# Kernel optimization log

Measured on AMD Instinct MI355X. Metric: run time of the kernel, lower is better.

The kernel has to match this reference:

```python
import jax, jax.numpy as jnp
import numpy as np

N_NODES = 20000
BN_EPS = 1e-5


def setup_inputs() -> dict:
    key = jax.random.key(0)
    ks = jax.random.split(key, 8)
    in_dim, half, out_dim, n_edges = 256, 128, 256, 320000
    s = 1.0 / np.sqrt(in_dim)
    return {
        "x": jax.random.normal(ks[0], (N_NODES, in_dim), dtype=jnp.float32),
        "edge_index": jax.random.randint(ks[1], (2, n_edges), 0, N_NODES, dtype=jnp.int64),
        "W_l_f": jax.random.normal(ks[2], (half, in_dim), dtype=jnp.float32) * s,
        "b_l_f": jnp.zeros((half,), dtype=jnp.float32),
        "W_r_f": jax.random.normal(ks[3], (half, in_dim), dtype=jnp.float32) * s,
        "W_l_b": jax.random.normal(ks[4], (half, in_dim), dtype=jnp.float32) * s,
        "b_l_b": jnp.zeros((half,), dtype=jnp.float32),
        "W_r_b": jax.random.normal(ks[5], (half, in_dim), dtype=jnp.float32) * s,
        "gamma": jnp.ones((out_dim,), dtype=jnp.float32),
        "beta": jnp.zeros((out_dim,), dtype=jnp.float32),
    }


def _sage(x, src, dst, W_l, b_l, W_r):
    # mean-aggregate source features at destination nodes (PyG SAGEConv, aggr='mean')
    msg_sum = jax.ops.segment_sum(x[src], dst, num_segments=N_NODES)
    cnt = jax.ops.segment_sum(jnp.ones((src.shape[0],), x.dtype), dst, num_segments=N_NODES)
    aggr = msg_sum / jnp.maximum(cnt, 1.0)[:, None]
    # lin_l(aggr) + lin_r(x); lin_l carries the bias in PyG
    return aggr @ W_l.T + b_l + x @ W_r.T


def reference(x, edge_index, W_l_f, b_l_f, W_r_f, W_l_b, b_l_b, W_r_b, gamma, beta):
    src, dst = edge_index[0], edge_index[1]
    h_fwd = _sage(x, src, dst, W_l_f, b_l_f, W_r_f)
    h_bwd = _sage(x, dst, src, W_l_b, b_l_b, W_r_b)  # flipped edges
    h = jnp.concatenate([h_fwd, h_bwd], axis=-1)  # [N, out_dim]
    # BatchNorm1d in training mode (N > 1), biased variance
    mean = jnp.mean(h, axis=0)
    var = jnp.mean(jnp.square(h - mean), axis=0)
    h = (h - mean) * jax.lax.rsqrt(var + BN_EPS) * gamma + beta
    return jax.nn.relu(h)
```

## Files before the change

### kernel.cpp

```cpp
#include <hip/hip_runtime.h>
#include <hip/hip_bf16.h>

#define N_NODES 20000
#define N_EDGES 320000
#define BN_EPS  1e-5f

#define GEMM_MT  ((N_NODES + 127) / 128)
#define NGEMM    (GEMM_MT * 4)
#define FILLB    625

typedef __attribute__((ext_vector_type(4))) float f32x4;
typedef __attribute__((ext_vector_type(8))) __bf16 bf16x8;
typedef __attribute__((ext_vector_type(4))) unsigned short u16x4;

__device__ __forceinline__ unsigned short f2bf(float f) {
    unsigned int u = __float_as_uint(f);
    u += 0x7fffu + ((u >> 16) & 1u);
    return (unsigned short)(u >> 16);
}
__device__ __forceinline__ float bflo(unsigned int u) { return __uint_as_float(u << 16); }
__device__ __forceinline__ float bfhi(unsigned int u) { return __uint_as_float(u & 0xffff0000u); }

__device__ __forceinline__ void gload_lds16(const void* g, void* l) {
    __builtin_amdgcn_global_load_lds(
        (const __attribute__((address_space(1))) void*)g,
        (__attribute__((address_space(3))) void*)l, 16, 0, 0);
}

__global__ __launch_bounds__(256) void cvt_zero_kernel(
    const float* __restrict__ x,
    const float* __restrict__ Wlf, const float* __restrict__ Wlb,
    const float* __restrict__ Wrf, const float* __restrict__ Wrb,
    unsigned short* __restrict__ Xb, unsigned short* __restrict__ Wb,
    uint4* __restrict__ zp, int zquads)
{
    const int XQ = N_NODES * 256 / 4;
    const int WQ = 128 * 256 / 4;
    const int total = XQ + 4 * WQ + zquads;
    for (int i = blockIdx.x * blockDim.x + threadIdx.x; i < total; i += gridDim.x * blockDim.x) {
        if (i >= XQ + 4 * WQ) {
            zp[i - XQ - 4 * WQ] = make_uint4(0, 0, 0, 0);
            continue;
        }
        const float* sp;
        unsigned short* dp;
        if (i < XQ) {
            sp = x + (size_t)i * 4;
            dp = Xb + (size_t)i * 4;
        } else {
            int w = i - XQ;
            int mat = w / WQ;
            int o = (w - mat * WQ) * 4;
            if      (mat == 0) sp = Wlf + o;
            else if (mat == 1) sp = Wlb + o;
            else if (mat == 2) sp = Wrf + o;
            else               sp = Wrb + o;
            dp = Wb + (size_t)mat * 32768 + o;
        }
        float4 v = *(const float4*)sp;
        u16x4 r = {f2bf(v.x), f2bf(v.y), f2bf(v.z), f2bf(v.w)};
        *(u16x4*)dp = r;
    }
}

__global__ void count_rank_kernel(const int* __restrict__ src, const int* __restrict__ dst,
                                  int* __restrict__ cntF, int* __restrict__ cntB,
                                  unsigned int* __restrict__ rank2) {
    int e = blockIdx.x * blockDim.x + threadIdx.x;
    if (e < N_EDGES) {
        unsigned int p = (unsigned int)atomicAdd(&cntF[dst[e]], 1);
        unsigned int q = (unsigned int)atomicAdd(&cntB[src[e]], 1);
        rank2[e] = p | (q << 16);
    }
}

#define SCAN_PER 20
__global__ __launch_bounds__(1024) void scan_kernel(const int* __restrict__ cntF, int* __restrict__ offF,
                                                    const int* __restrict__ cntB, int* __restrict__ offB) {
    const int* in  = blockIdx.x ? cntB : cntF;
    int*       out = blockIdx.x ? offB : offF;
    int t = threadIdx.x;
    int base = t * SCAN_PER;
    int v[SCAN_PER];
    int sum = 0;
    #pragma unroll
    for (int k = 0; k < SCAN_PER; ++k) {
        int i = base + k;
        int c = (i < N_NODES) ? in[i] : 0;
        v[k] = sum; sum += c;
    }
    __shared__ int sh[1024];
    sh[t] = sum;
    __syncthreads();
    for (int o = 1; o < 1024; o <<= 1) {
        int x = (t >= o) ? sh[t - o] : 0;
        __syncthreads();
        sh[t] += x;
        __syncthreads();
    }
    int pre = t ? sh[t - 1] : 0;
    #pragma unroll
    for (int k = 0; k < SCAN_PER; ++k) {
        int i = base + k;
        if (i < N_NODES) out[i] = pre + v[k];
    }
    if (t == 1023) out[N_NODES] = sh[1023];
}

__global__ __launch_bounds__(256) void gemm_fill_kernel(
    const int* __restrict__ src, const int* __restrict__ dst,
    const int* __restrict__ offF, const int* __restrict__ offB,
    const unsigned int* __restrict__ rank2,
    int* __restrict__ listF, int* __restrict__ listB,
    const unsigned short* __restrict__ Xb, const unsigned short* __restrict__ Wb,
    unsigned short* __restrict__ Y, float* __restrict__ Z)
{
    __shared__ unsigned short As[2][128 * 64];
    __shared__ unsigned short Bs[2][128 * 64];

    if (blockIdx.x >= NGEMM) {
        int t = (blockIdx.x - NGEMM) * 256 + threadIdx.x;
        #pragma unroll
        for (int h = 0; h < 2; ++h) {
            int e = t + h * (N_EDGES / 2);
            int s = src[e], d = dst[e];
            unsigned int r2 = rank2[e];
            listF[offF[d] + (int)(r2 & 0xffffu)] = s;
            listB[offB[s] + (int)(r2 >> 16)] = d;
        }
        return;
    }

    int gb = blockIdx.x;
    int by = gb & 3;
    int mBase = (gb >> 2) * 128;
    int tid = threadIdx.x, lane = tid & 63, wave = tid >> 6;
    int wr = wave >> 1, wc = wave & 1;
    const unsigned short* W = Wb + (size_t)by * 128 * 256;

    f32x4 acc[4][4] = {};

    auto STAGE = [&](int b, int k0) {
        #pragma unroll
        for (int c = 0; c < 4; ++c) {
            int S = c * 256 + tid;
            int row = S >> 3;
            int q = (S & 7) ^ (row & 7);
            int gm = mBase + row; gm = gm < N_NODES ? gm : N_NODES - 1;
            gload_lds16(Xb + (size_t)gm * 256 + k0 + q * 8, &As[b][S * 8]);
            gload_lds16(W + (size_t)row * 256 + k0 + q * 8, &Bs[b][S * 8]);
        }
    };
    auto COMPUTE = [&](int b) {
        #pragma unroll
        for (int ks = 0; ks < 2; ++ks) {
            bf16x8 af[4], bfr[4];
            int sl = ks * 4 + (lane >> 4);
            #pragma unroll
            for (int m = 0; m < 4; ++m) {
                int row = wr * 64 + m * 16 + (lane & 15);
                af[m] = *(const bf16x8*)&As[b][row * 64 + ((sl ^ (row & 7)) * 8)];
            }
            #pragma unroll
            for (int n = 0; n < 4; ++n) {
                int row = wc * 64 + n * 16 + (lane & 15);
                bfr[n] = *(const bf16x8*)&Bs[b][row * 64 + ((sl ^ (row & 7)) * 8)];
            }
            #pragma unroll
            for (int m = 0; m < 4; ++m)
                #pragma unroll
                for (int n = 0; n < 4; ++n)
                    acc[m][n] = __builtin_amdgcn_mfma_f32_16x16x32_bf16(af[m], bfr[n], acc[m][n], 0, 0, 0);
        }
    };

    STAGE(0, 0);
    #pragma unroll
    for (int t = 0; t < 4; ++t) {
        if (t < 3) {
            STAGE((t + 1) & 1, (t + 1) * 64);
            asm volatile("s_waitcnt vmcnt(8)" ::: "memory");
        } else {
            asm volatile("s_waitcnt vmcnt(0)" ::: "memory");
        }
        __builtin_amdgcn_s_barrier();
        __builtin_amdgcn_sched_barrier(0);
        COMPUTE(t & 1);
        __builtin_amdgcn_s_barrier();
    }

    bool toY = by < 2;
    int cBase = (by & 1) * 128 + wc * 64;
    #pragma unroll
    for (int m = 0; m < 4; ++m) {
        int gm0 = mBase + wr * 64 + m * 16 + (lane >> 4) * 4;
        #pragma unroll
        for (int n = 0; n < 4; ++n) {
            int gn = cBase + n * 16 + (lane & 15);
            f32x4 v = acc[m][n];
            #pragma unroll
            for (int j = 0; j < 4; ++j) {
                int gm = gm0 + j;
                if (gm < N_NODES) {
                    if (toY) Y[(size_t)gm * 256 + gn] = f2bf(v[j]);
                    else     Z[(size_t)gm * 256 + gn] = v[j];
                }
            }
        }
    }
}

#define NPW 2
__global__ __launch_bounds__(256) void aggregate_kernel(
    const unsigned short* __restrict__ Y,
    const int* __restrict__ offF, const int* __restrict__ listF,
    const int* __restrict__ offB, const int* __restrict__ listB,
    float* __restrict__ H)
{
    int tid = threadIdx.x, lane = tid & 63, wave = tid >> 6;
    int dir = wave >> 1, half = wave & 1;
    const int* off  = dir ? offB : offF;
    const int* list = dir ? listB : listF;
    int eg = lane >> 4;
    int c16 = lane & 15;
    int nodeBase = blockIdx.x * (2 * NPW) + half * NPW;

    for (int jn = 0; jn < NPW; ++jn) {
        int n = nodeBase + jn;
        int beg = off[n], end = off[n + 1];
        int deg = end - beg;
        float acc[8] = {0.f, 0.f, 0.f, 0.f, 0.f, 0.f, 0.f, 0.f};

        for (int i = beg; i < end; i += 64) {
            int c = end - i; if (c > 64) c = 64;
            int u_l = list[i + (lane < c ? lane : 0)];
            for (int e0 = 0; e0 < c; e0 += 16) {
                uint4 v[4];
                #pragma unroll
                for (int k = 0; k < 4; ++k) {
                    int ei = e0 + k * 4 + eg;
                    int u = __shfl(u_l, ei < c ? ei : 0);
                    v[k] = make_uint4(0u, 0u, 0u, 0u);
                    if (ei < c)
                        v[k] = *(const uint4*)(Y + (size_t)u * 256 + dir * 128 + c16 * 8);
                }
                #pragma unroll
                for (int k = 0; k < 4; ++k) {
                    acc[0] += bflo(v[k].x); acc[1] += bfhi(v[k].x);
                    acc[2] += bflo(v[k].y); acc[3] += bfhi(v[k].y);
                    acc[4] += bflo(v[k].z); acc[5] += bfhi(v[k].z);
                    acc[6] += bflo(v[k].w); acc[7] += bfhi(v[k].w);
                }
            }
        }
        #pragma unroll
        for (int j = 0; j < 8; ++j) {
            acc[j] += __shfl_xor(acc[j], 16);
            acc[j] += __shfl_xor(acc[j], 32);
        }
        float h0 = (eg & 2) ? ((eg & 1) ? acc[6] : acc[4]) : ((eg & 1) ? acc[2] : acc[0]);
        float h1 = (eg & 2) ? ((eg & 1) ? acc[7] : acc[5]) : ((eg & 1) ? acc[3] : acc[1]);
        float inv = 1.f / fmaxf((float)deg, 1.f);
        float2* hp = (float2*)(H + (size_t)n * 256 + dir * 128 + c16 * 8 + eg * 2);
        float2 z = *hp;
        *hp = make_float2(fmaf(h0, inv, z.x), fmaf(h1, inv, z.y));
    }
}

__global__ __launch_bounds__(256) void bn_stats_kernel(const float* __restrict__ H,
                                                       float* __restrict__ stats) {
    int col = threadIdx.x;
    float s1 = 0.f, s2 = 0.f;
    for (int n = blockIdx.x; n < N_NODES; n += gridDim.x) {
        float h = H[(size_t)n * 256 + col];
        s1 += h;
        s2 += h * h;
    }
    atomicAdd(&stats[col], s1);
    atomicAdd(&stats[256 + col], s2);
}

__global__ __launch_bounds__(256) void bn_kernel(
    const float* __restrict__ stats, const float* __restrict__ gamma,
    const float* __restrict__ beta, float* __restrict__ H)
{
    __shared__ float sc[256], sf[256];
    int tid = threadIdx.x;
    {
        float mean = stats[tid] * (1.f / N_NODES);
        float var  = stats[256 + tid] * (1.f / N_NODES) - mean * mean;
        float s = rsqrtf(fmaxf(var, 0.f) + BN_EPS) * gamma[tid];
        sc[tid] = s;
        sf[tid] = beta[tid] - mean * s;
    }
    __syncthreads();
    for (int n = blockIdx.x; n < N_NODES; n += gridDim.x) {
        size_t idx = (size_t)n * 256 + tid;
        float h = H[idx];
        H[idx] = fmaxf(h * sc[tid] + sf[tid], 0.f);
    }
}

extern "C" void kernel_launch(void* const* d_in, const int* in_sizes, int n_in,
                              void* d_out, int out_size, void* d_ws, size_t ws_size,
                              hipStream_t stream) {
    const float* x     = (const float*)d_in[0];
    const int*   edge  = (const int*)d_in[1];
    const float* Wlf   = (const float*)d_in[2];
    const float* Wrf   = (const float*)d_in[4];
    const float* Wlb   = (const float*)d_in[5];
    const float* Wrb   = (const float*)d_in[7];
    const float* gamma = (const float*)d_in[8];
    const float* beta  = (const float*)d_in[9];
    float* out = (float*)d_out;

    const int* src = edge;
    const int* dst = edge + N_EDGES;

    char* ws = (char*)d_ws;
    size_t off = 0;
    auto alloc = [&](size_t bytes) { size_t r = off; off += (bytes + 255) & ~(size_t)255; return r; };
    unsigned short* Y  = (unsigned short*)(ws + alloc((size_t)N_NODES * 256 * 2));
    unsigned short* Xb = (unsigned short*)(ws + alloc((size_t)N_NODES * 256 * 2));
    unsigned short* Wb = (unsigned short*)(ws + alloc((size_t)4 * 128 * 256 * 2));
    int* offF  = (int*)(ws + alloc((size_t)(N_NODES + 1) * 4));
    int* offB  = (int*)(ws + alloc((size_t)(N_NODES + 1) * 4));
    int* listF = (int*)(ws + alloc((size_t)N_EDGES * 4));
    int* listB = (int*)(ws + alloc((size_t)N_EDGES * 4));
    unsigned int* rank2 = (unsigned int*)(ws + alloc((size_t)N_EDGES * 4));
    size_t zbase_off = off;
    int* cntF = (int*)(ws + alloc((size_t)N_NODES * 4));
    int* cntB = (int*)(ws + alloc((size_t)N_NODES * 4));
    float* stats = (float*)(ws + alloc(512 * 4));
    size_t zbytes = off - zbase_off;

    cvt_zero_kernel<<<2048, 256, 0, stream>>>(x, Wlf, Wlb, Wrf, Wrb, Xb, Wb,
                                              (uint4*)(ws + zbase_off), (int)(zbytes / 16));

    count_rank_kernel<<<(N_EDGES + 255) / 256, 256, 0, stream>>>(src, dst, cntF, cntB, rank2);
    scan_kernel<<<2, 1024, 0, stream>>>(cntF, offF, cntB, offB);

    gemm_fill_kernel<<<NGEMM + FILLB, 256, 0, stream>>>(
        src, dst, offF, offB, rank2, listF, listB, Xb, Wb, Y, out);

    aggregate_kernel<<<N_NODES / (2 * NPW), 256, 0, stream>>>(
        Y, offF, listF, offB, listB, out);

    bn_stats_kernel<<<512, 256, 0, stream>>>(out, stats);
    bn_kernel<<<2048, 256, 0, stream>>>(stats, gamma, beta, out);
}
```

Baseline: 131.6 us.

## Fuse BN statistics into aggregation and merge conversion with edge counting

The BN column sums and sums of squares are now accumulated inside the aggregation kernel. Each block reduces its partials in shared memory and atomically adds them into one of 8 striped stat buffers, which removes the separate pass that re-read all of H. The bf16 conversion and the edge count/rank kernels are merged into a single launch, and zeroing moves to its own small kernel launched first. The fusion adds 4 atomics per thread-column per block (5000 blocks spread over 8 copies), which risks atomic contention, and the per-block stats partials are float sums.

```diff
diff --git a/kernel.cpp b/kernel.cpp
--- a/kernel.cpp
+++ b/kernel.cpp
@@ -5,9 +5,12 @@
 #define N_EDGES 320000
 #define BN_EPS  1e-5f
 
+#define CVTB2    2048
+#define CNT256   1250
 #define GEMM_MT  ((N_NODES + 127) / 128)
 #define NGEMM    (GEMM_MT * 4)
 #define FILLB    625
+#define NSTATS   8
 
 typedef __attribute__((ext_vector_type(4))) float f32x4;
 typedef __attribute__((ext_vector_type(8))) __bf16 bf16x8;
@@ -27,46 +30,48 @@
         (__attribute__((address_space(3))) void*)l, 16, 0, 0);
 }
 
-__global__ __launch_bounds__(256) void cvt_zero_kernel(
+__global__ void zero_kernel(uint4* __restrict__ zp, int n) {
+    int i = blockIdx.x * blockDim.x + threadIdx.x;
+    if (i < n) zp[i] = make_uint4(0u, 0u, 0u, 0u);
+}
+
+__global__ __launch_bounds__(256) void cvt_count_kernel(
     const float* __restrict__ x,
     const float* __restrict__ Wlf, const float* __restrict__ Wlb,
     const float* __restrict__ Wrf, const float* __restrict__ Wrb,
     unsigned short* __restrict__ Xb, unsigned short* __restrict__ Wb,
-    uint4* __restrict__ zp, int zquads)
+    const int* __restrict__ src, const int* __restrict__ dst,
+    int* __restrict__ cntF, int* __restrict__ cntB,
+    unsigned int* __restrict__ rank2)
 {
-    const int XQ = N_NODES * 256 / 4;
-    const int WQ = 128 * 256 / 4;
-    const int total = XQ + 4 * WQ + zquads;
-    for (int i = blockIdx.x * blockDim.x + threadIdx.x; i < total; i += gridDim.x * blockDim.x) {
-        if (i >= XQ + 4 * WQ) {
-            zp[i - XQ - 4 * WQ] = make_uint4(0, 0, 0, 0);
-            continue;
-        }
-        const float* sp;
-        unsigned short* dp;
-        if (i < XQ) {
-            sp = x + (size_t)i * 4;
-            dp = Xb + (size_t)i * 4;
-        } else {
-            int w = i - XQ;
-            int mat = w / WQ;
-            int o = (w - mat * WQ) * 4;
-            if      (mat == 0) sp = Wlf + o;
-            else if (mat == 1) sp = Wlb + o;
-            else if (mat == 2) sp = Wrf + o;
-            else               sp = Wrb + o;
-            dp = Wb + (size_t)mat * 32768 + o;
-        }
-        float4 v = *(const float4*)sp;
-        u16x4 r = {f2bf(v.x), f2bf(v.y), f2bf(v.z), f2bf(v.w)};
-        *(u16x4*)dp = r;
-    }
-}
-
-__global__ void count_rank_kernel(const int* __restrict__ src, const int* __restrict__ dst,
-                                  int* __restrict__ cntF, int* __restrict__ cntB,
-                                  unsigned int* __restrict__ rank2) {
-    int e = blockIdx.x * blockDim.x + threadIdx.x;
+    int tid = threadIdx.x;
+    if (blockIdx.x < CVTB2) {
+        const int XQ = N_NODES * 256 / 4;
+        const int WQ = 128 * 256 / 4;
+        const int total = XQ + 4 * WQ;
+        for (int i = blockIdx.x * 256 + tid; i < total; i += CVTB2 * 256) {
+            const float* sp;
+            unsigned short* dp;
+            if (i < XQ) {
+                sp = x + (size_t)i * 4;
+                dp = Xb + (size_t)i * 4;
+            } else {
+                int w = i - XQ;
+                int mat = w / WQ;
+                int o = (w - mat * WQ) * 4;
+                if      (mat == 0) sp = Wlf + o;
+                else if (mat == 1) sp = Wlb + o;
+                else if (mat == 2) sp = Wrf + o;
+                else               sp = Wrb + o;
+                dp = Wb + (size_t)mat * 32768 + o;
+            }
+            float4 v = *(const float4*)sp;
+            u16x4 r = {f2bf(v.x), f2bf(v.y), f2bf(v.z), f2bf(v.w)};
+            *(u16x4*)dp = r;
+        }
+        return;
+    }
+    int e = (blockIdx.x - CVTB2) * 256 + tid;
     if (e < N_EDGES) {
         unsigned int p = (unsigned int)atomicAdd(&cntF[dst[e]], 1);
         unsigned int q = (unsigned int)atomicAdd(&cntB[src[e]], 1);
@@ -211,11 +216,11 @@
 }
 
 #define NPW 2
-__global__ __launch_bounds__(256) void aggregate_kernel(
+__global__ __launch_bounds__(256) void aggregate_stats_kernel(
     const unsigned short* __restrict__ Y,
     const int* __restrict__ offF, const int* __restrict__ listF,
     const int* __restrict__ offB, const int* __restrict__ listB,
-    float* __restrict__ H)
+    float* __restrict__ H, float* __restrict__ stats)
 {
     int tid = threadIdx.x, lane = tid & 63, wave = tid >> 6;
     int dir = wave >> 1, half = wave & 1;
@@ -224,6 +229,8 @@
     int eg = lane >> 4;
     int c16 = lane & 15;
     int nodeBase = blockIdx.x * (2 * NPW) + half * NPW;
+
+    float s1a = 0.f, s1b = 0.f, s2a = 0.f, s2b = 0.f;
 
     for (int jn = 0; jn < NPW; ++jn) {
         int n = nodeBase + jn;
@@ -263,21 +270,29 @@
         float inv = 1.f / fmaxf((float)deg, 1.f);
         float2* hp = (float2*)(H + (size_t)n * 256 + dir * 128 + c16 * 8 + eg * 2);
         float2 z = *hp;
-        *hp = make_float2(fmaf(h0, inv, z.x), fmaf(h1, inv, z.y));
-    }
-}
-
-__global__ __launch_bounds__(256) void bn_stats_kernel(const float* __restrict__ H,
-                                                       float* __restrict__ stats) {
-    int col = threadIdx.x;
-    float s1 = 0.f, s2 = 0.f;
-    for (int n = blockIdx.x; n < N_NODES; n += gridDim.x) {
-        float h = H[(size_t)n * 256 + col];
-        s1 += h;
-        s2 += h * h;
-    }
-    atomicAdd(&stats[col], s1);
-    atomicAdd(&stats[256 + col], s2);
+        float v0 = fmaf(h0, inv, z.x);
+        float v1 = fmaf(h1, inv, z.y);
+        *hp = make_float2(v0, v1);
+        s1a += v0; s2a += v0 * v0;
+        s1b += v1; s2b += v1 * v1;
+    }
+
+    __shared__ float red[2][64][4];
+    if (half) {
+        red[dir][lane][0] = s1a; red[dir][lane][1] = s1b;
+        red[dir][lane][2] = s2a; red[dir][lane][3] = s2b;
+    }
+    __syncthreads();
+    if (!half) {
+        s1a += red[dir][lane][0]; s1b += red[dir][lane][1];
+        s2a += red[dir][lane][2]; s2b += red[dir][lane][3];
+        int col = dir * 128 + c16 * 8 + eg * 2;
+        float* st = stats + (blockIdx.x & (NSTATS - 1)) * 512;
+        atomicAdd(&st[col], s1a);
+        atomicAdd(&st[col + 1], s1b);
+        atomicAdd(&st[256 + col], s2a);
+        atomicAdd(&st[256 + col + 1], s2b);
+    }
 }
 
 __global__ __launch_bounds__(256) void bn_kernel(
@@ -287,8 +302,14 @@
     __shared__ float sc[256], sf[256];
     int tid = threadIdx.x;
     {
-        float mean = stats[tid] * (1.f / N_NODES);
-        float var  = stats[256 + tid] * (1.f / N_NODES) - mean * mean;
+        float s1 = 0.f, s2 = 0.f;
+        #pragma unroll
+        for (int c = 0; c < NSTATS; ++c) {
+            s1 += stats[c * 512 + tid];
+            s2 += stats[c * 512 + 256 + tid];
+        }
+        float mean = s1 * (1.f / N_NODES);
+        float var  = s2 * (1.f / N_NODES) - mean * mean;
         float s = rsqrtf(fmaxf(var, 0.f) + BN_EPS) * gamma[tid];
         sc[tid] = s;
         sf[tid] = beta[tid] - mean * s;
@@ -331,21 +352,22 @@
     size_t zbase_off = off;
     int* cntF = (int*)(ws + alloc((size_t)N_NODES * 4));
     int* cntB = (int*)(ws + alloc((size_t)N_NODES * 4));
-    float* stats = (float*)(ws + alloc(512 * 4));
+    float* stats = (float*)(ws + alloc((size_t)NSTATS * 512 * 4));
     size_t zbytes = off - zbase_off;
-
-    cvt_zero_kernel<<<2048, 256, 0, stream>>>(x, Wlf, Wlb, Wrf, Wrb, Xb, Wb,
-                                              (uint4*)(ws + zbase_off), (int)(zbytes / 16));
-
-    count_rank_kernel<<<(N_EDGES + 255) / 256, 256, 0, stream>>>(src, dst, cntF, cntB, rank2);
+    int zquads = (int)(zbytes / 16);
+
+    zero_kernel<<<(zquads + 255) / 256, 256, 0, stream>>>((uint4*)(ws + zbase_off), zquads);
+
+    cvt_count_kernel<<<CVTB2 + CNT256, 256, 0, stream>>>(
+        x, Wlf, Wlb, Wrf, Wrb, Xb, Wb, src, dst, cntF, cntB, rank2);
+
     scan_kernel<<<2, 1024, 0, stream>>>(cntF, offF, cntB, offB);
 
     gemm_fill_kernel<<<NGEMM + FILLB, 256, 0, stream>>>(
         src, dst, offF, offB, rank2, listF, listB, Xb, Wb, Y, out);
 
-    aggregate_kernel<<<N_NODES / (2 * NPW), 256, 0, stream>>>(
-        Y, offF, listF, offB, listB, out);
-
-    bn_stats_kernel<<<512, 256, 0, stream>>>(out, stats);
+    aggregate_stats_kernel<<<N_NODES / (2 * NPW), 256, 0, stream>>>(
+        Y, offF, listF, offB, listB, out, stats);
+
     bn_kernel<<<2048, 256, 0, stream>>>(stats, gamma, beta, out);
 }
```

Measured after the change: 132.4 us. No clear change (+0.6%).
